# Optimization experiments

Measured on AMD Instinct MI355X. Metric: run time of the kernel, lower is better.

Reference implementation:

```python
import jax, jax.numpy as jnp
import numpy as np

FEA = 14      # feature_scal
OUT = 7       # adaptive pool output size
SCALE = 1.0 / 16.0


def _axis_weights(start, end, size):
    """Adaptive-avg-pool weights along one axis for a slice [start, end).
    Matches torch AdaptiveAvgPool1d bin edges: s_i = floor(i*L/OUT),
    e_i = ceil((i+1)*L/OUT). Returns [OUT, size] averaging matrix."""
    i = jnp.arange(OUT)
    length = end - start
    s = start + (i * length) // OUT
    e = start + ((i + 1) * length + (OUT - 1)) // OUT  # ceil div
    pos = jnp.arange(size)
    m = (pos[None, :] >= s[:, None]) & (pos[None, :] < e[:, None])
    denom = jnp.maximum(e - s, 1).astype(jnp.float32)
    return m.astype(jnp.float32) / denom[:, None]


def setup_inputs() -> dict:
    key = jax.random.key(0)
    k1, k2, k3, k4, k5 = jax.random.split(key, 5)
    B, C, N = 1, 2048, 512
    tensor = jax.random.normal(k1, (B, C, FEA, FEA), dtype=jnp.float32)
    # ROI rows: [batch_idx, x1, y1, x2, y2] in 224x224 image pixels
    x1 = jax.random.uniform(k2, (N,), minval=0.0, maxval=120.0)
    y1 = jax.random.uniform(k3, (N,), minval=0.0, maxval=120.0)
    w = jax.random.uniform(k4, (N,), minval=32.0, maxval=100.0)
    h = jax.random.uniform(k5, (N,), minval=32.0, maxval=100.0)
    x2 = jnp.minimum(x1 + w, 224.0)
    y2 = jnp.minimum(y1 + h, 224.0)
    ROI = jnp.stack([jnp.zeros((N,)), x1, y1, x2, y2], axis=1).astype(jnp.float32)
    return {"tensor": tensor, "ROI": ROI}


def reference(tensor, ROI):
    # Scale coords to feature-map space; floor/clip starts, ceil/clip ends
    c = ROI[:, 1:] * SCALE  # [N,4] = x1,y1,x2,y2
    x1 = jnp.clip(jnp.floor(c[:, 0]), 0, FEA).astype(jnp.int32)
    y1 = jnp.clip(jnp.floor(c[:, 1]), 0, FEA).astype(jnp.int32)
    x2 = jnp.clip(jnp.ceil(c[:, 2]), 0, FEA).astype(jnp.int32)
    y2 = jnp.clip(jnp.ceil(c[:, 3]), 0, FEA).astype(jnp.int32)
    Wy = jax.vmap(lambda a, b: _axis_weights(a, b, FEA))(y1, y2)  # [N,7,H]
    Wx = jax.vmap(lambda a, b: _axis_weights(a, b, FEA))(x1, x2)  # [N,7,W]
    # pooled[n,b,c,i,j] = sum_{y,x} Wy[n,i,y] * tensor[b,c,y,x] * Wx[n,j,x]
    out = jnp.einsum('niy,bcyx,njx->nbcij', Wy, tensor, Wx)
    N, B, C = out.shape[:3]
    return out.reshape(N * B, C, OUT, OUT)
```

## Files before the change

### kernel.cpp

```cpp
#include <hip/hip_runtime.h>

#define FEA    14
#define OUT    7
#define SCALE  (1.0f / 16.0f)
#define BLK    256
#define CMAX   7
#define RS     17
#define CH     (15 * RS)
#define GROUPS 16

#define C7P 0.14295714f
#define C7M 0.14275714f

__device__ __forceinline__ float inv_small(int d) {
    return (d <= 1) ? 1.0f : ((d == 2) ? 0.5f : 0.33333334f);
}

__global__ __launch_bounds__(BLK) void roi_adaptive_pool_kernel(
    const float* __restrict__ tensor,
    const float* __restrict__ ROI,
    float* __restrict__ out,
    int C, int N)
{
    __shared__ float S[CMAX * CH];

    const int tid   = threadIdx.x;
    const int o0    = blockIdx.x * BLK;
    const int total = C * OUT * OUT;

    const int c_lo = o0 / 49;
    const int c_hi = min((o0 + BLK - 1) / 49, C - 1);
    const int cnt  = c_hi - c_lo + 1;

    if (tid < CMAX * FEA) {
        const int cl = tid / FEA;
        const int y  = tid - cl * FEA;
        if (cl < cnt) {
            const float* __restrict__ g =
                tensor + (size_t)(c_lo + cl) * (FEA * FEA) + y * FEA;
            float* __restrict__ s = &S[cl * CH + (y + 1) * RS];
            s[0] = 0.f;
            float run = 0.f;
#pragma unroll
            for (int x = 0; x < FEA; ++x) { run += g[x]; s[x + 1] = run; }
        }
    } else if (tid < CMAX * FEA + CMAX * 15) {
        const int t2 = tid - CMAX * FEA;
        const int cl = t2 / 15;
        const int x  = t2 - cl * 15;
        if (cl < cnt) S[cl * CH + x] = 0.f;
    }
    __syncthreads();

    if (tid < CMAX * FEA) {
        const int cl = tid / FEA;
        const int x  = (tid - cl * FEA) + 1;
        if (cl < cnt) {
            float* __restrict__ s = &S[cl * CH + x];
            float run = 0.f;
#pragma unroll
            for (int y = 1; y <= FEA; ++y) { run += s[y * RS]; s[y * RS] = run; }
        }
    }

    const int oi = o0 + tid;
    const bool active = (oi < total);
    const int c  = active ? (oi / 49) : c_lo;
    const int rr = active ? (oi - c * 49) : 0;
    const int i  = rr / 7;
    const int j  = rr - i * 7;
    const int sb = (c - c_lo) * CH;
    const float jP  = (float)j       * C7P;
    const float j1M = (float)(j + 1) * C7M;
    const float iP  = (float)i       * C7P;
    const float i1M = (float)(i + 1) * C7M;

    __syncthreads();

    const int per   = (N + GROUPS - 1) / GROUPS;
    const int n0    = blockIdx.y * per;
    const int n_end = min(n0 + per, N);
    if (n0 >= n_end) return;

    float* __restrict__ outp = out + (size_t)n0 * total + oi;
    float rx1 = ROI[(size_t)n0 * 5 + 1], ry1 = ROI[(size_t)n0 * 5 + 2];
    float rx2 = ROI[(size_t)n0 * 5 + 3], ry2 = ROI[(size_t)n0 * 5 + 4];

    for (int n = n0; n < n_end; ++n) {
        const float x1f = floorf(rx1 * SCALE);
        const float y1f = floorf(ry1 * SCALE);
        const float x2f = ceilf (rx2 * SCALE);
        const float y2f = ceilf (ry2 * SCALE);
        if (n + 1 < n_end) {
            const float* __restrict__ rp = &ROI[(size_t)(n + 1) * 5];
            rx1 = rp[1]; ry1 = rp[2]; rx2 = rp[3]; ry2 = rp[4];
        }
        const float Lxf = x2f - x1f;
        const float Lyf = y2f - y1f;
        const int x1i = (int)x1f, y1i = (int)y1f;

        const int sx = x1i + (int)(jP * Lxf);
        const int ex = x1i + (int)ceilf(j1M * Lxf);
        const int sy = y1i + (int)(iP * Lyf);
        const int ey = y1i + (int)ceilf(i1M * Lyf);
        const float w = inv_small(ex - sx) * inv_small(ey - sy);

        const float* __restrict__ Sy0 = &S[sb + sy * RS];
        const float* __restrict__ Sy1 = &S[sb + ey * RS];
        const float acc = (Sy1[ex] - Sy0[ex]) - (Sy1[sx] - Sy0[sx]);

        if (active) __builtin_nontemporal_store(acc * w, outp);
        outp += total;
    }
}

extern "C" void kernel_launch(void* const* d_in, const int* in_sizes, int n_in,
                              void* d_out, int out_size, void* d_ws, size_t ws_size,
                              hipStream_t stream) {
    const float* tensor = (const float*)d_in[0];
    const float* ROI    = (const float*)d_in[1];
    float*       out    = (float*)d_out;

    const int C = in_sizes[0] / (FEA * FEA);
    const int N = in_sizes[1] / 5;

    const int total = C * OUT * OUT;
    dim3 block(BLK, 1, 1);
    dim3 grid((total + BLK - 1) / BLK, GROUPS, 1);
    roi_adaptive_pool_kernel<<<grid, block, 0, stream>>>(tensor, ROI, out, C, N);
}
```

Measured before the change: 232.2 us.

## Precompute packed per-ROI bin table in a separate kernel

Adds a small pre-pass kernel that computes each ROI's 49 bin boundaries and averaging weights once and packs them into a uint2 table in the workspace. The main kernel then loads one record per output bin instead of recomputing floor/ceil and multiplies per thread for every channel. This removes redundant per-channel index arithmetic but adds a second launch and a table read from global/L2 per iteration. When the workspace is too small, the old single-kernel path is used instead.

```diff
diff --git a/kernel.cpp b/kernel.cpp
--- a/kernel.cpp
+++ b/kernel.cpp
@@ -1,4 +1,5 @@
 #include <hip/hip_runtime.h>
+#include <stdint.h>
 
 #define FEA    14
 #define OUT    7
@@ -16,9 +17,36 @@
     return (d <= 1) ? 1.0f : ((d == 2) ? 0.5f : 0.33333334f);
 }
 
-__global__ __launch_bounds__(BLK) void roi_adaptive_pool_kernel(
+__global__ __launch_bounds__(BLK) void roi_bins_kernel(
+    const float* __restrict__ ROI, uint2* __restrict__ tab, int N)
+{
+    const int k = blockIdx.x * BLK + threadIdx.x;
+    if (k >= N * 49) return;
+    const int n  = k / 49;
+    const int ij = k - n * 49;
+    const int i  = ij / 7;
+    const int j  = ij - i * 7;
+    const float* __restrict__ r = &ROI[(size_t)n * 5];
+    const int x1i = (int)floorf(r[1] * SCALE);
+    const int y1i = (int)floorf(r[2] * SCALE);
+    const int x2i = (int)ceilf (r[3] * SCALE);
+    const int y2i = (int)ceilf (r[4] * SCALE);
+    const int Lx = x2i - x1i, Ly = y2i - y1i;
+    const int sx = x1i + (j * Lx) / 7;
+    const int ex = x1i + ((j + 1) * Lx + 6) / 7;
+    const int sy = y1i + (i * Ly) / 7;
+    const int ey = y1i + ((i + 1) * Ly + 6) / 7;
+    const float w = inv_small(ex - sx) * inv_small(ey - sy);
+    uint2 rec;
+    rec.x = (uint32_t)sx | ((uint32_t)ex << 8)
+          | ((uint32_t)(sy * RS) << 16) | ((uint32_t)(ey * RS) << 24);
+    rec.y = __float_as_uint(w);
+    tab[k] = rec;
+}
+
+__global__ __launch_bounds__(BLK) void roi_pool_main(
     const float* __restrict__ tensor,
-    const float* __restrict__ ROI,
+    const uint2* __restrict__ tab,
     float* __restrict__ out,
     int C, int N)
 {
@@ -63,6 +91,76 @@
         }
     }
 
+    const int oi = o0 + tid;
+    const bool active = (oi < total);
+    const int c  = active ? (oi / 49) : c_lo;
+    const int ij = active ? (oi - c * 49) : 0;
+    const float* __restrict__ Sc = S + (c - c_lo) * CH;
+
+    __syncthreads();
+
+    const int per   = (N + GROUPS - 1) / GROUPS;
+    const int n0    = blockIdx.y * per;
+    const int n_end = min(n0 + per, N);
+    if (n0 >= n_end) return;
+
+    float* __restrict__ outp = out + (size_t)n0 * total + oi;
+    int ridx = n0 * 49 + ij;
+    uint2 rec = tab[ridx];
+    for (int n = n0; n < n_end; ++n) {
+        const uint32_t p = rec.x;
+        const float    w = __uint_as_float(rec.y);
+        if (n + 1 < n_end) rec = tab[ridx + 49];
+        ridx += 49;
+        const int sx  =  p        & 0xFF;
+        const int ex  = (p >> 8)  & 0xFF;
+        const int oy0 = (p >> 16) & 0xFF;
+        const int oy1 =  p >> 24;
+        const float acc = (Sc[oy1 + ex] - Sc[oy0 + ex]) - (Sc[oy1 + sx] - Sc[oy0 + sx]);
+        if (active) __builtin_nontemporal_store(acc * w, outp);
+        outp += total;
+    }
+}
+
+__global__ __launch_bounds__(BLK) void roi_pool_fallback(
+    const float* __restrict__ tensor, const float* __restrict__ ROI,
+    float* __restrict__ out, int C, int N)
+{
+    __shared__ float S[CMAX * CH];
+    const int tid   = threadIdx.x;
+    const int o0    = blockIdx.x * BLK;
+    const int total = C * OUT * OUT;
+    const int c_lo = o0 / 49;
+    const int c_hi = min((o0 + BLK - 1) / 49, C - 1);
+    const int cnt  = c_hi - c_lo + 1;
+    if (tid < CMAX * FEA) {
+        const int cl = tid / FEA;
+        const int y  = tid - cl * FEA;
+        if (cl < cnt) {
+            const float* __restrict__ g = tensor + (size_t)(c_lo + cl) * (FEA * FEA) + y * FEA;
+            float* __restrict__ s = &S[cl * CH + (y + 1) * RS];
+            s[0] = 0.f;
+            float run = 0.f;
+#pragma unroll
+            for (int x = 0; x < FEA; ++x) { run += g[x]; s[x + 1] = run; }
+        }
+    } else if (tid < CMAX * FEA + CMAX * 15) {
+        const int t2 = tid - CMAX * FEA;
+        const int cl = t2 / 15;
+        const int x  = t2 - cl * 15;
+        if (cl < cnt) S[cl * CH + x] = 0.f;
+    }
+    __syncthreads();
+    if (tid < CMAX * FEA) {
+        const int cl = tid / FEA;
+        const int x  = (tid - cl * FEA) + 1;
+        if (cl < cnt) {
+            float* __restrict__ s = &S[cl * CH + x];
+            float run = 0.f;
+#pragma unroll
+            for (int y = 1; y <= FEA; ++y) { run += s[y * RS]; s[y * RS] = run; }
+        }
+    }
     const int oi = o0 + tid;
     const bool active = (oi < total);
     const int c  = active ? (oi / 49) : c_lo;
@@ -74,18 +172,14 @@
     const float j1M = (float)(j + 1) * C7M;
     const float iP  = (float)i       * C7P;
     const float i1M = (float)(i + 1) * C7M;
-
-    __syncthreads();
-
+    __syncthreads();
     const int per   = (N + GROUPS - 1) / GROUPS;
     const int n0    = blockIdx.y * per;
     const int n_end = min(n0 + per, N);
     if (n0 >= n_end) return;
-
     float* __restrict__ outp = out + (size_t)n0 * total + oi;
     float rx1 = ROI[(size_t)n0 * 5 + 1], ry1 = ROI[(size_t)n0 * 5 + 2];
     float rx2 = ROI[(size_t)n0 * 5 + 3], ry2 = ROI[(size_t)n0 * 5 + 4];
-
     for (int n = n0; n < n_end; ++n) {
         const float x1f = floorf(rx1 * SCALE);
         const float y1f = floorf(ry1 * SCALE);
@@ -98,17 +192,14 @@
         const float Lxf = x2f - x1f;
         const float Lyf = y2f - y1f;
         const int x1i = (int)x1f, y1i = (int)y1f;
-
         const int sx = x1i + (int)(jP * Lxf);
         const int ex = x1i + (int)ceilf(j1M * Lxf);
         const int sy = y1i + (int)(iP * Lyf);
         const int ey = y1i + (int)ceilf(i1M * Lyf);
         const float w = inv_small(ex - sx) * inv_small(ey - sy);
-
         const float* __restrict__ Sy0 = &S[sb + sy * RS];
         const float* __restrict__ Sy1 = &S[sb + ey * RS];
         const float acc = (Sy1[ex] - Sy0[ex]) - (Sy1[sx] - Sy0[sx]);
-
         if (active) __builtin_nontemporal_store(acc * w, outp);
         outp += total;
     }
@@ -127,5 +218,14 @@
     const int total = C * OUT * OUT;
     dim3 block(BLK, 1, 1);
     dim3 grid((total + BLK - 1) / BLK, GROUPS, 1);
-    roi_adaptive_pool_kernel<<<grid, block, 0, stream>>>(tensor, ROI, out, C, N);
-}
+
+    const size_t tab_bytes = (size_t)N * 49 * sizeof(uint2);
+    if (ws_size >= tab_bytes) {
+        uint2* tab = (uint2*)d_ws;
+        const int nbins = N * 49;
+        roi_bins_kernel<<<(nbins + BLK - 1) / BLK, block, 0, stream>>>(ROI, tab, N);
+        roi_pool_main<<<grid, block, 0, stream>>>(tensor, tab, out, C, N);
+    } else {
+        roi_pool_fallback<<<grid, block, 0, stream>>>(tensor, ROI, out, C, N);
+    }
+}
```

New measurement: 227.4 us. 2.1% less time.
